# Kernel optimization log

Measured on AMD Instinct MI355X. Metric: run time of the kernel, lower is better.

## Reference

```python
import jax, jax.numpy as jnp
import numpy as np
from jax.scipy.special import digamma, gammaln

B, N, H, W, D = 16, 1024, 32, 32, 256
TEMP = 0.5
KL_WEIGHT = 1e-3


def setup_inputs() -> dict:
    key = jax.random.key(0)
    k1, k2, k3 = jax.random.split(key, 3)
    logits = jax.random.normal(k1, (B, N, H, W), dtype=jnp.float32)
    # codebook initialized uniform(-1/N, 1/N) as in init_type == 'uniform'
    codebook = jax.random.uniform(k2, (N, D), dtype=jnp.float32,
                                  minval=-1.0 / N, maxval=1.0 / N)
    # uniform noise for the Gumbel-softmax rsample (channels-last layout [B,H,W,N])
    uniform_noise = jax.random.uniform(k3, (B, H, W, N), dtype=jnp.float32,
                                       minval=1e-6, maxval=1.0 - 1e-6)
    return {"logits": logits, "codebook": codebook, "uniform_noise": uniform_noise}


def reference(logits, codebook, uniform_noise):
    # convert_to_alpha: evidential mapping alpha = softplus(logits) + 1,
    # then permute(0,2,3,1) -> [B, H, W, N]
    alpha = jax.nn.softplus(jnp.transpose(logits, (0, 2, 3, 1))) + 1.0
    S = jnp.sum(alpha, axis=-1, keepdims=True)            # [B,H,W,1]
    probs = alpha / S                                      # [B,H,W,N]

    # RelaxedOneHotCategorical(temp, probs).rsample() == Gumbel-softmax
    gumbel = -jnp.log(-jnp.log(uniform_noise))
    sample = jax.nn.softmax((jnp.log(probs) + gumbel) / TEMP, axis=-1)  # [B,H,W,N]

    vector_weights = jnp.transpose(sample, (0, 3, 1, 2))   # [B,N,H,W]
    indices = jnp.argmax(vector_weights, axis=1)           # [B,H,W]

    # quantized output via codebook combine
    z_q = jnp.einsum('bnhw,nd->bdhw', vector_weights, codebook)  # [B,D,H,W]

    # KL( Dirichlet(alpha) || Dirichlet(ones(N)) ), closed form with beta=1:
    # lgamma(S) - sum lgamma(alpha) - lgamma(N) + sum (alpha-1)*(digamma(alpha)-digamma(S))
    S1 = S[..., 0]
    kl = (gammaln(S1)
          - jnp.sum(gammaln(alpha), axis=-1)
          - gammaln(jnp.float32(N))
          + jnp.sum((alpha - 1.0) * (digamma(alpha) - digamma(S)), axis=-1))
    kl_loss = KL_WEIGHT * jnp.mean(kl)

    # perplexity over soft encodings
    avg_probs = jnp.mean(sample.reshape(-1, N), axis=0)
    perplexity = jnp.exp(-jnp.sum(avg_probs * jnp.log(avg_probs + 1e-10)))

    return (z_q, kl_loss, indices, perplexity)
```

## Files before the change

### kernel.cpp

```cpp
#include <hip/hip_runtime.h>
#include <math.h>

#define NB 16
#define NN 1024
#define NH 32
#define NW 32
#define ND 256
#define NPIX (NB*NH*NW)

#define ZQ_OFF  0
#define KL_OFF  4194304
#define IDX_OFF 4194305
#define PPL_OFF 4210689

#define LGAMMA_1024F 6071.2804f
#define BS_ROW_B 2080

typedef _Float16 f16x8 __attribute__((ext_vector_type(8)));
typedef _Float16 f16x4 __attribute__((ext_vector_type(4)));
typedef float    f32x4 __attribute__((ext_vector_type(4)));
typedef float    f32x2 __attribute__((ext_vector_type(2)));

__device__ __forceinline__ float fast_rcp(float x){ return __builtin_amdgcn_rcpf(x); }

__device__ __forceinline__ f32x2 elem2(f32x2 x, f32x2 u,
                                       f32x2& S, f32x2& L, f32x2& P,
                                       f32x2& prodAcc){
    f32x2 t;   t[0] = __expf(-fabsf(x[0]));  t[1] = __expf(-fabsf(x[1]));
    f32x2 mx0; mx0[0] = fmaxf(x[0], 0.f);    mx0[1] = fmaxf(x[1], 0.f);
    f32x2 l1p; l1p[0] = __logf(1.f + t[0]);  l1p[1] = __logf(1.f + t[1]);
    f32x2 a  = mx0 + l1p + 1.f;
    f32x2 a1 = a + 1.f, a2 = a + 2.f, z = a + 3.f;
    f32x2 t12  = a1*a2;
    f32x2 prod = a*t12;
    f32x2 rz;  rz[0] = fast_rcp(z[0]);       rz[1] = fast_rcp(z[1]);
    f32x2 rp;  rp[0] = fast_rcp(prod[0]);    rp[1] = fast_rcp(prod[1]);
    f32x2 lz;  lz[0] = __logf(z[0]);         lz[1] = __logf(z[1]);
    prodAcc = prodAcc * prod;
    f32x2 rz2 = rz*rz;
    f32x2 lg = (z - 0.5f)*lz - z + 0.918938533f
             + rz*(0.083333333f - 0.002777778f*rz2);
    f32x2 sr = (t12 + a*(a + a + 3.f))*rp;
    f32x2 dg = lz - 0.5f*rz - rz2*(0.083333333f - 0.008333333f*rz2) - sr;
    S += a; L += lg; P += (a - 1.f)*dg;
    f32x2 d = 1.f - u;
    f32x2 lup = -d*(1.f + d*(0.5f + d*(0.33333333f + d*(0.25f
              + d*(0.2f + d*(0.16666667f + d*0.14285714f))))));
    f32x2 lu;
    lu[0] = (d[0] < 0.09f) ? lup[0] : __logf(u[0]);
    lu[1] = (d[1] < 0.09f) ? lup[1] : __logf(u[1]);
    f32x2 ar; ar[0] = a[0]*fast_rcp(lu[0]);  ar[1] = a[1]*fast_rcp(lu[1]);
    return ar*ar;
}

__global__ __launch_bounds__(256) void k_tr(
    const float* __restrict__ cb, _Float16* __restrict__ cbT)
{
    const int kb = blockIdx.x, kq = blockIdx.y, d = threadIdx.x;
    _Float16 tmp[8];
#pragma unroll
    for (int i = 0; i < 8; ++i)
        tmp[i] = (_Float16)cb[(size_t)(32*kb + 8*kq + i)*ND + d];
    *(f16x8*)(cbT + (size_t)kb*8192 + (size_t)d*32 + 8*kq) = *(f16x8*)tmp;
}

__global__ __launch_bounds__(1024, 2) void k_mega(
    const float* __restrict__ logits, const float* __restrict__ noise,
    const _Float16* __restrict__ cbT, float* __restrict__ colpart,
    float* __restrict__ klpart, float* __restrict__ out)
{
    __shared__ __align__(16) char lds[16*BS_ROW_B + 6*256*4];
    char*  bsb  = lds;
    float* redS = (float*)(lds + 16*BS_ROW_B);
    float* redL = redS + 256;
    float* redP = redL + 256;
    float* redZ = redP + 256;
    float* redM = redZ + 256;
    int*   redI = (int*)(redM + 256);

    const int t    = threadIdx.x;
    const int row  = blockIdx.x >> 1;
    const int w0   = (blockIdx.x & 1) * 16;
    const int b    = row >> 5, h = row & 31;
    const int lane = t & 63;
    const int v    = t >> 6;
    const int wl   = lane & 15;
    const int j4   = (lane >> 4) & 3;
    const int p    = row*32 + w0 + wl;
    const int nq   = 4*v + j4;

    const float* lgB = logits + (size_t)b*(NN*NH*NW) + (size_t)(4*nq)*(NH*NW)
                     + (size_t)h*NW + w0 + wl;
    const float* nzB = noise  + (size_t)p*NN + 4*nq;

    f32x4 u0, u1, u2, u3;
    float x00,x01,x02,x03, x10,x11,x12,x13;
    float x20,x21,x22,x23, x30,x31,x32,x33;
    float ev[16];
    f32x2 SA = (f32x2)0.f, LA = (f32x2)0.f, PA = (f32x2)0.f, ZA = (f32x2)0.f;
    f32x2 SB = (f32x2)0.f, LB = (f32x2)0.f, PB = (f32x2)0.f, ZB = (f32x2)0.f;
    f32x2 prA = (f32x2)1.f, prB = (f32x2)1.f;
    float mxA = -1.f, mxB = -1.f;
    int   idxA = 0, idxB = 0;

    asm volatile(
        "global_load_dwordx4 %0, %4, off\n\t"
        "global_load_dwordx4 %1, %4, off offset:1024\n\t"
        "global_load_dwordx4 %2, %4, off offset:2048\n\t"
        "global_load_dwordx4 %3, %4, off offset:3072"
        : "=&v"(u0), "=&v"(u1), "=&v"(u2), "=&v"(u3)
        : "v"(nzB));

#define LG_ASM(X0,X1,X2,X3,KK) \
    asm volatile( \
        "global_load_dword %0, %4, off offset:-4096\n\t" \
        "global_load_dword %1, %4, off\n\t" \
        "global_load_dword %2, %5, off offset:-4096\n\t" \
        "global_load_dword %3, %5, off" \
        : "=&v"(X0), "=&v"(X1), "=&v"(X2), "=&v"(X3) \
        : "v"(lgB + (size_t)(256*(KK))*1024 + 1024), \
          "v"(lgB + (size_t)(256*(KK))*1024 + 3072))

    LG_ASM(x00,x01,x02,x03, 0);
    LG_ASM(x10,x11,x12,x13, 1);
    LG_ASM(x20,x21,x22,x23, 2);
    LG_ASM(x30,x31,x32,x33, 3);
#undef LG_ASM

#define WAITV(NSTR) do{ asm volatile("s_waitcnt vmcnt(" NSTR ")"); \
                        __builtin_amdgcn_sched_barrier(0); }while(0)

#define DO_PAIR(kk, X0,X1,X2,X3, UV) do{                          \
    f32x2 xA_, xB_, uA_, uB_;                                     \
    xA_[0]=X0; xA_[1]=X1; xB_[0]=X2; xB_[1]=X3;                   \
    uA_[0]=UV[0]; uA_[1]=UV[1]; uB_[0]=UV[2]; uB_[1]=UV[3];       \
    f32x2 eA = elem2(xA_, uA_, SA, LA, PA, prA);                  \
    f32x2 eB = elem2(xB_, uB_, SB, LB, PB, prB);                  \
    ZA += eA; ZB += eB;                                           \
    if (eA[0] > mxA){ mxA = eA[0]; idxA = 256*(kk) + 4*nq + 0; }  \
    if (eA[1] > mxA){ mxA = eA[1]; idxA = 256*(kk) + 4*nq + 1; }  \
    if (eB[0] > mxB){ mxB = eB[0]; idxB = 256*(kk) + 4*nq + 2; }  \
    if (eB[1] > mxB){ mxB = eB[1]; idxB = 256*(kk) + 4*nq + 3; }  \
    ev[4*(kk)+0]=eA[0]; ev[4*(kk)+1]=eA[1];                       \
    ev[4*(kk)+2]=eB[0]; ev[4*(kk)+3]=eB[1]; }while(0)

    WAITV("12");
    DO_PAIR(0, x00,x01,x02,x03, u0);
    WAITV("8");
    DO_PAIR(1, x10,x11,x12,x13, u1);
    WAITV("4");
    DO_PAIR(2, x20,x21,x22,x23, u2);
    WAITV("0");
    DO_PAIR(3, x30,x31,x32,x33, u3);
#undef WAITV
#undef DO_PAIR

    float S = (SA[0] + SA[1]) + (SB[0] + SB[1]);
    float L = (LA[0] + LA[1]) + (LB[0] + LB[1])
            - __logf(prA[0]*prA[1]) - __logf(prB[0]*prB[1]);
    float P = (PA[0] + PA[1]) + (PB[0] + PB[1]);
    float Z = (ZA[0] + ZA[1]) + (ZB[0] + ZB[1]);
    float mx; int idx;
    {
        bool take = (mxB > mxA) || (mxB == mxA && idxB < idxA);
        mx  = take ? mxB : mxA;
        idx = take ? idxB : idxA;
    }

#pragma unroll
    for (int mask = 16; mask < 64; mask <<= 1){
        S += __shfl_xor(S, mask);
        L += __shfl_xor(L, mask);
        P += __shfl_xor(P, mask);
        Z += __shfl_xor(Z, mask);
        float mo = __shfl_xor(mx, mask);
        int   io = __shfl_xor(idx, mask);
        bool take = (mo > mx) || (mo == mx && io < idx);
        mx  = take ? mo : mx;
        idx = take ? io : idx;
    }
    if (j4 == 0){
        redS[16*v + wl] = S;  redL[16*v + wl] = L;
        redP[16*v + wl] = P;  redZ[16*v + wl] = Z;
        redM[16*v + wl] = mx; redI[16*v + wl] = idx;
    }
    __syncthreads();

    float Zt = 0.f;
#pragma unroll
    for (int qz = 0; qz < 16; ++qz) Zt += redZ[16*qz + wl];
    const float zinv = fast_rcp(Zt);

    {
        char* brow = bsb + wl*BS_ROW_B;
        const int sw   = wl & 7;
        const int sub8 = (nq & 1) << 3;
        const int cb2  = nq >> 1;
#pragma unroll
        for (int k = 0; k < 4; ++k){
            f16x4 hv;
            hv[0] = (_Float16)(ev[4*k+0]*zinv);
            hv[1] = (_Float16)(ev[4*k+1]*zinv);
            hv[2] = (_Float16)(ev[4*k+2]*zinv);
            hv[3] = (_Float16)(ev[4*k+3]*zinv);
            *(f16x4*)(brow + (((32*k + cb2) ^ sw) << 4) + sub8) = hv;
        }
    }
    __syncthreads();

    const _Float16* aBase = cbT + (size_t)(16*v + wl)*32 + j4*8;
    const char* bRow = bsb + wl*BS_ROW_B;
    const int fsw = wl & 7;

    f32x4 acc = (f32x4)0.f;
    f16x8 ar[4];
    ar[0] = *(const f16x8*)(aBase);
    ar[1] = *(const f16x8*)(aBase + 8192);
    ar[2] = *(const f16x8*)(aBase + 2*8192);

#pragma unroll
    for (int kb = 0; kb < 32; ++kb){
        if (kb + 3 < 32)
            ar[(kb+3)&3] = *(const f16x8*)(aBase + (size_t)(kb+3)*8192);
        f16x8 bf = *(const f16x8*)(bRow + ((((kb << 2) | j4) ^ fsw) << 4));
        acc = __builtin_amdgcn_mfma_f32_16x16x32_f16(ar[kb&3], bf, acc, 0, 0, 0);
    }

    float* outp = out + (size_t)b*(ND*1024) + h*32 + w0;
#pragma unroll
    for (int r = 0; r < 4; ++r){
        int d = 16*v + 4*j4 + r;
        outp[(size_t)d*1024 + wl] = acc[r];
    }

    {
        float s0 = 0.f;
#pragma unroll
        for (int r = 0; r < 16; ++r){
            const char* br = bsb + r*BS_ROW_B;
            const int sw2 = r & 7;
            s0 += (float)*(const _Float16*)(br + ((((t >> 3) ^ sw2) << 4) + 2*(t & 7)));
        }
        colpart[(size_t)blockIdx.x*NN + t] = s0;
    }

    if (t < 16){
        float Sq = 0.f, Lq = 0.f, Pq = 0.f, M = -1.f;
        int I = 0x7fffffff;
#pragma unroll
        for (int qz = 0; qz < 16; ++qz){
            Sq += redS[16*qz + t]; Lq += redL[16*qz + t]; Pq += redP[16*qz + t];
            float m = redM[16*qz + t]; int i = redI[16*qz + t];
            bool take = (m > M) || (m == M && i < I);
            M = take ? m : M; I = take ? i : I;
        }
        out[IDX_OFF + row*32 + w0 + t] = (float)I;
        float rS  = fast_rcp(Sq);
        float lnS = __logf(Sq);
        float lgS = (Sq - 0.5f)*lnS - Sq + 0.918938533f + 0.083333333f*rS;
        float dgS = lnS - 0.5f*rS;
        float kl = lgS - Lq - LGAMMA_1024F + (Pq - dgS*(Sq - 1024.f));
#pragma unroll
        for (int mask = 1; mask < 16; mask <<= 1) kl += __shfl_xor(kl, mask);
        if (t == 0) klpart[blockIdx.x] = kl;
    }
}

__global__ __launch_bounds__(256) void k_red(
    const float* __restrict__ colpart, float* __restrict__ colsum)
{
    __shared__ float red[8][32];
    const int nl = threadIdx.x & 31;
    const int rs = threadIdx.x >> 5;
    const int n  = blockIdx.x*32 + nl;
    const float* cp = colpart + (size_t)rs*128*NN + n;
    float s = 0.f;
#pragma unroll 8
    for (int r = 0; r < 128; ++r)
        s += cp[(size_t)r*NN];
    red[rs][nl] = s;
    __syncthreads();
    if (threadIdx.x < 32){
        float tot = 0.f;
#pragma unroll
        for (int i = 0; i < 8; ++i) tot += red[i][threadIdx.x];
        colsum[blockIdx.x*32 + threadIdx.x] = tot;
    }
}

__global__ __launch_bounds__(256) void k_final(
    const float* __restrict__ colsum, const float* __restrict__ klpart,
    float* __restrict__ out)
{
    __shared__ float red[8];
    const int tid = threadIdx.x;
    float s = 0.f, kls = 0.f;
#pragma unroll
    for (int n = tid; n < NN; n += 256){
        float avg = colsum[n] * (1.f/16384.f);
        s += avg * logf(avg + 1e-10f);
        kls += klpart[n];
    }
#pragma unroll
    for (int mask = 1; mask < 64; mask <<= 1){
        s   += __shfl_xor(s, mask);
        kls += __shfl_xor(kls, mask);
    }
    if ((tid & 63) == 0){ red[tid >> 6] = s; red[4 + (tid >> 6)] = kls; }
    __syncthreads();
    if (tid == 0){
        float tot = red[0] + red[1] + red[2] + red[3];
        float klt = red[4] + red[5] + red[6] + red[7];
        out[PPL_OFF] = expf(-tot);
        out[KL_OFF]  = 1e-3f * (klt * (1.f/16384.f));
    }
}

extern "C" void kernel_launch(void* const* d_in, const int* in_sizes, int n_in,
                              void* d_out, int out_size, void* d_ws, size_t ws_size,
                              hipStream_t stream)
{
    const float* logits = (const float*)d_in[0];
    const float* cb     = (const float*)d_in[1];
    const float* noise  = (const float*)d_in[2];
    float* out = (float*)d_out;

    float* colpart = (float*)d_ws;
    float* colsum  = colpart + (size_t)1024*NN;
    float* klpart  = colsum + NN;
    _Float16* cbT  = (_Float16*)(klpart + NN);

    k_tr   <<<dim3(32, 4), 256, 0, stream>>>(cb, cbT);
    k_mega <<<dim3(1024), 1024, 0, stream>>>(logits, noise, cbT, colpart, klpart, out);
    k_red  <<<dim3(32),    256, 0, stream>>>(colpart, colsum);
    k_final<<<1, 256, 0, stream>>>(colsum, klpart, out);
}
```

Measured before the change: 214.0 us.

## Process two half-rows per block with prefetch overlap and shared codebook fragments

Each block now handles a full 32-pixel row as two 16-pixel halves. The second half's noise and logits loads are issued before the first half's LDS barrier and softmax write, so their memory latency overlaps the first half's reduction. In the MFMA loop, each codebook fragment loaded from global memory feeds two accumulators, halving cbT traffic per pixel. The grid is halved and the colpart/klpart reductions shrink to match. The cost is more registers and LDS per block, with launch_bounds raised to 8 that may force spills.

```diff
diff --git a/kernel.cpp b/kernel.cpp
--- a/kernel.cpp
+++ b/kernel.cpp
@@ -53,6 +53,23 @@
     return ar*ar;
 }
 
+__device__ __forceinline__ void bs_write(char* bsb, int wl, int nq,
+                                         const float* ev, float zinv){
+    char* brow = bsb + wl*BS_ROW_B;
+    const int sw   = wl & 7;
+    const int sub8 = (nq & 1) << 3;
+    const int cb2  = nq >> 1;
+#pragma unroll
+    for (int k = 0; k < 4; ++k){
+        f16x4 hv;
+        hv[0] = (_Float16)(ev[4*k+0]*zinv);
+        hv[1] = (_Float16)(ev[4*k+1]*zinv);
+        hv[2] = (_Float16)(ev[4*k+2]*zinv);
+        hv[3] = (_Float16)(ev[4*k+3]*zinv);
+        *(f16x4*)(brow + (((32*k + cb2) ^ sw) << 4) + sub8) = hv;
+    }
+}
+
 __global__ __launch_bounds__(256) void k_tr(
     const float* __restrict__ cb, _Float16* __restrict__ cbT)
 {
@@ -64,71 +81,76 @@
     *(f16x8*)(cbT + (size_t)kb*8192 + (size_t)d*32 + 8*kq) = *(f16x8*)tmp;
 }
 
-__global__ __launch_bounds__(1024, 2) void k_mega(
+__global__ __launch_bounds__(1024, 8) void k_mega(
     const float* __restrict__ logits, const float* __restrict__ noise,
     const _Float16* __restrict__ cbT, float* __restrict__ colpart,
     float* __restrict__ klpart, float* __restrict__ out)
 {
-    __shared__ __align__(16) char lds[16*BS_ROW_B + 6*256*4];
-    char*  bsb  = lds;
-    float* redS = (float*)(lds + 16*BS_ROW_B);
-    float* redL = redS + 256;
-    float* redP = redL + 256;
-    float* redZ = redP + 256;
-    float* redM = redZ + 256;
-    int*   redI = (int*)(redM + 256);
+    __shared__ __align__(16) char lds[32*BS_ROW_B + 12*256*4];
+    char*  bsb0 = lds;
+    char*  bsb1 = lds + 16*BS_ROW_B;
+    float* redB = (float*)(lds + 32*BS_ROW_B);
 
     const int t    = threadIdx.x;
-    const int row  = blockIdx.x >> 1;
-    const int w0   = (blockIdx.x & 1) * 16;
-    const int b    = row >> 5, h = row & 31;
+    const int row  = blockIdx.x;
+    const int b    = row >> 5, hh = row & 31;
     const int lane = t & 63;
     const int v    = t >> 6;
     const int wl   = lane & 15;
     const int j4   = (lane >> 4) & 3;
-    const int p    = row*32 + w0 + wl;
     const int nq   = 4*v + j4;
 
-    const float* lgB = logits + (size_t)b*(NN*NH*NW) + (size_t)(4*nq)*(NH*NW)
-                     + (size_t)h*NW + w0 + wl;
-    const float* nzB = noise  + (size_t)p*NN + 4*nq;
+    const float* lgB0 = logits + (size_t)b*(NN*NH*NW) + (size_t)(4*nq)*(NH*NW)
+                      + (size_t)hh*NW + wl;
+    const float* nzB0 = noise  + (size_t)(row*32 + wl)*NN + 4*nq;
+    const float* lgB1 = lgB0 + 16;
+    const float* nzB1 = nzB0 + (size_t)16*NN;
+
+    float ev[16];
+    f32x2 SA, LA, PA, ZA, SB, LB, PB, ZB, prA, prB;
+    float mxA, mxB;
+    int   idxA, idxB;
 
     f32x4 u0, u1, u2, u3;
     float x00,x01,x02,x03, x10,x11,x12,x13;
     float x20,x21,x22,x23, x30,x31,x32,x33;
-    float ev[16];
-    f32x2 SA = (f32x2)0.f, LA = (f32x2)0.f, PA = (f32x2)0.f, ZA = (f32x2)0.f;
-    f32x2 SB = (f32x2)0.f, LB = (f32x2)0.f, PB = (f32x2)0.f, ZB = (f32x2)0.f;
-    f32x2 prA = (f32x2)1.f, prB = (f32x2)1.f;
-    float mxA = -1.f, mxB = -1.f;
-    int   idxA = 0, idxB = 0;
-
-    asm volatile(
-        "global_load_dwordx4 %0, %4, off\n\t"
-        "global_load_dwordx4 %1, %4, off offset:1024\n\t"
-        "global_load_dwordx4 %2, %4, off offset:2048\n\t"
-        "global_load_dwordx4 %3, %4, off offset:3072"
-        : "=&v"(u0), "=&v"(u1), "=&v"(u2), "=&v"(u3)
-        : "v"(nzB));
-
-#define LG_ASM(X0,X1,X2,X3,KK) \
+    f32x4 w0, w1, w2, w3;
+    float y00,y01,y02,y03, y10,y11,y12,y13;
+    float y20,y21,y22,y23, y30,y31,y32,y33;
+
+#define NZ_ASM(U0,U1,U2,U3, NZP) \
+    asm volatile( \
+        "global_load_dwordx4 %0, %4, off\n\t" \
+        "global_load_dwordx4 %1, %4, off offset:1024\n\t" \
+        "global_load_dwordx4 %2, %4, off offset:2048\n\t" \
+        "global_load_dwordx4 %3, %4, off offset:3072" \
+        : "=&v"(U0), "=&v"(U1), "=&v"(U2), "=&v"(U3) : "v"(NZP))
+
+#define LG_ASM(X0,X1,X2,X3, LGP, KK) \
     asm volatile( \
         "global_load_dword %0, %4, off offset:-4096\n\t" \
         "global_load_dword %1, %4, off\n\t" \
         "global_load_dword %2, %5, off offset:-4096\n\t" \
         "global_load_dword %3, %5, off" \
         : "=&v"(X0), "=&v"(X1), "=&v"(X2), "=&v"(X3) \
-        : "v"(lgB + (size_t)(256*(KK))*1024 + 1024), \
-          "v"(lgB + (size_t)(256*(KK))*1024 + 3072))
-
-    LG_ASM(x00,x01,x02,x03, 0);
-    LG_ASM(x10,x11,x12,x13, 1);
-    LG_ASM(x20,x21,x22,x23, 2);
-    LG_ASM(x30,x31,x32,x33, 3);
-#undef LG_ASM
+        : "v"((LGP) + (size_t)(256*(KK))*1024 + 1024), \
+          "v"((LGP) + (size_t)(256*(KK))*1024 + 3072))
 
 #define WAITV(NSTR) do{ asm volatile("s_waitcnt vmcnt(" NSTR ")"); \
                         __builtin_amdgcn_sched_barrier(0); }while(0)
+
+#define BARRIER() do{ \
+    __builtin_amdgcn_sched_barrier(0); \
+    asm volatile("s_waitcnt lgkmcnt(0)" ::: "memory"); \
+    __builtin_amdgcn_sched_barrier(0); \
+    __builtin_amdgcn_s_barrier(); \
+    __builtin_amdgcn_sched_barrier(0); }while(0)
+
+#define STATS_INIT() do{ \
+    SA = (f32x2)0.f; LA = (f32x2)0.f; PA = (f32x2)0.f; ZA = (f32x2)0.f; \
+    SB = (f32x2)0.f; LB = (f32x2)0.f; PB = (f32x2)0.f; ZB = (f32x2)0.f; \
+    prA = (f32x2)1.f; prB = (f32x2)1.f; \
+    mxA = -1.f; mxB = -1.f; idxA = 0; idxB = 0; }while(0)
 
 #define DO_PAIR(kk, X0,X1,X2,X3, UV) do{                          \
     f32x2 xA_, xB_, uA_, uB_;                                     \
@@ -144,126 +166,159 @@
     ev[4*(kk)+0]=eA[0]; ev[4*(kk)+1]=eA[1];                       \
     ev[4*(kk)+2]=eB[0]; ev[4*(kk)+3]=eB[1]; }while(0)
 
-    WAITV("12");
-    DO_PAIR(0, x00,x01,x02,x03, u0);
-    WAITV("8");
-    DO_PAIR(1, x10,x11,x12,x13, u1);
-    WAITV("4");
-    DO_PAIR(2, x20,x21,x22,x23, u2);
-    WAITV("0");
-    DO_PAIR(3, x30,x31,x32,x33, u3);
-#undef WAITV
-#undef DO_PAIR
-
-    float S = (SA[0] + SA[1]) + (SB[0] + SB[1]);
-    float L = (LA[0] + LA[1]) + (LB[0] + LB[1])
-            - __logf(prA[0]*prA[1]) - __logf(prB[0]*prB[1]);
-    float P = (PA[0] + PA[1]) + (PB[0] + PB[1]);
-    float Z = (ZA[0] + ZA[1]) + (ZB[0] + ZB[1]);
-    float mx; int idx;
+#define REDUCE_STORE(BANK) do{                                    \
+    float S = (SA[0]+SA[1]) + (SB[0]+SB[1]);                      \
+    float L = (LA[0]+LA[1]) + (LB[0]+LB[1])                       \
+            - __logf(prA[0]*prA[1]) - __logf(prB[0]*prB[1]);      \
+    float P = (PA[0]+PA[1]) + (PB[0]+PB[1]);                      \
+    float Z = (ZA[0]+ZA[1]) + (ZB[0]+ZB[1]);                      \
+    float mx; int idx;                                            \
+    { bool take = (mxB > mxA) || (mxB == mxA && idxB < idxA);     \
+      mx = take ? mxB : mxA; idx = take ? idxB : idxA; }          \
+    _Pragma("unroll")                                             \
+    for (int mask = 16; mask < 64; mask <<= 1){                   \
+        S += __shfl_xor(S, mask);                                 \
+        L += __shfl_xor(L, mask);                                 \
+        P += __shfl_xor(P, mask);                                 \
+        Z += __shfl_xor(Z, mask);                                 \
+        float mo = __shfl_xor(mx, mask);                          \
+        int   io = __shfl_xor(idx, mask);                         \
+        bool take = (mo > mx) || (mo == mx && io < idx);          \
+        mx = take ? mo : mx; idx = take ? io : idx;               \
+    }                                                             \
+    if (j4 == 0){                                                 \
+        float* bk = redB + (BANK)*1536;                           \
+        bk[       16*v + wl] = S;  bk[256  + 16*v + wl] = L;      \
+        bk[512  + 16*v + wl] = P;  bk[768  + 16*v + wl] = Z;      \
+        bk[1024 + 16*v + wl] = mx;                                \
+        ((int*)bk)[1280 + 16*v + wl] = idx;                       \
+    } }while(0)
+
+    NZ_ASM(u0,u1,u2,u3, nzB0);
+    LG_ASM(x00,x01,x02,x03, lgB0, 0);
+    LG_ASM(x10,x11,x12,x13, lgB0, 1);
+    LG_ASM(x20,x21,x22,x23, lgB0, 2);
+    LG_ASM(x30,x31,x32,x33, lgB0, 3);
+
+    STATS_INIT();
+    WAITV("12"); DO_PAIR(0, x00,x01,x02,x03, u0);
+    WAITV("8");  DO_PAIR(1, x10,x11,x12,x13, u1);
+    WAITV("4");  DO_PAIR(2, x20,x21,x22,x23, u2);
+    WAITV("0");  DO_PAIR(3, x30,x31,x32,x33, u3);
+    REDUCE_STORE(0);
+
+    NZ_ASM(w0,w1,w2,w3, nzB1);
+    LG_ASM(y00,y01,y02,y03, lgB1, 0);
+    LG_ASM(y10,y11,y12,y13, lgB1, 1);
+    LG_ASM(y20,y21,y22,y23, lgB1, 2);
+    LG_ASM(y30,y31,y32,y33, lgB1, 3);
+
+    BARRIER();
+
     {
-        bool take = (mxB > mxA) || (mxB == mxA && idxB < idxA);
-        mx  = take ? mxB : mxA;
-        idx = take ? idxB : idxA;
-    }
-
-#pragma unroll
-    for (int mask = 16; mask < 64; mask <<= 1){
-        S += __shfl_xor(S, mask);
-        L += __shfl_xor(L, mask);
-        P += __shfl_xor(P, mask);
-        Z += __shfl_xor(Z, mask);
-        float mo = __shfl_xor(mx, mask);
-        int   io = __shfl_xor(idx, mask);
-        bool take = (mo > mx) || (mo == mx && io < idx);
-        mx  = take ? mo : mx;
-        idx = take ? io : idx;
-    }
-    if (j4 == 0){
-        redS[16*v + wl] = S;  redL[16*v + wl] = L;
-        redP[16*v + wl] = P;  redZ[16*v + wl] = Z;
-        redM[16*v + wl] = mx; redI[16*v + wl] = idx;
-    }
-    __syncthreads();
-
-    float Zt = 0.f;
-#pragma unroll
-    for (int qz = 0; qz < 16; ++qz) Zt += redZ[16*qz + wl];
-    const float zinv = fast_rcp(Zt);
+        float Zt = 0.f;
+#pragma unroll
+        for (int q = 0; q < 16; ++q) Zt += redB[768 + 16*q + wl];
+        bs_write(bsb0, wl, nq, ev, fast_rcp(Zt));
+    }
+
+    STATS_INIT();
+    WAITV("12"); DO_PAIR(0, y00,y01,y02,y03, w0);
+    WAITV("8");  DO_PAIR(1, y10,y11,y12,y13, w1);
+    WAITV("4");  DO_PAIR(2, y20,y21,y22,y23, w2);
+    WAITV("0");  DO_PAIR(3, y30,y31,y32,y33, w3);
+    REDUCE_STORE(1);
+
+    BARRIER();
 
     {
-        char* brow = bsb + wl*BS_ROW_B;
-        const int sw   = wl & 7;
-        const int sub8 = (nq & 1) << 3;
-        const int cb2  = nq >> 1;
-#pragma unroll
-        for (int k = 0; k < 4; ++k){
-            f16x4 hv;
-            hv[0] = (_Float16)(ev[4*k+0]*zinv);
-            hv[1] = (_Float16)(ev[4*k+1]*zinv);
-            hv[2] = (_Float16)(ev[4*k+2]*zinv);
-            hv[3] = (_Float16)(ev[4*k+3]*zinv);
-            *(f16x4*)(brow + (((32*k + cb2) ^ sw) << 4) + sub8) = hv;
-        }
-    }
-    __syncthreads();
+        float Zt = 0.f;
+#pragma unroll
+        for (int q = 0; q < 16; ++q) Zt += redB[1536 + 768 + 16*q + wl];
+        bs_write(bsb1, wl, nq, ev, fast_rcp(Zt));
+    }
+
+    BARRIER();
 
     const _Float16* aBase = cbT + (size_t)(16*v + wl)*32 + j4*8;
-    const char* bRow = bsb + wl*BS_ROW_B;
+    const char* bRow0 = bsb0 + wl*BS_ROW_B;
+    const char* bRow1 = bsb1 + wl*BS_ROW_B;
     const int fsw = wl & 7;
 
-    f32x4 acc = (f32x4)0.f;
+    f32x4 acc0 = (f32x4)0.f, acc1 = (f32x4)0.f;
     f16x8 ar[4];
     ar[0] = *(const f16x8*)(aBase);
     ar[1] = *(const f16x8*)(aBase + 8192);
     ar[2] = *(const f16x8*)(aBase + 2*8192);
+    __builtin_amdgcn_sched_barrier(0);
 
 #pragma unroll
     for (int kb = 0; kb < 32; ++kb){
-        if (kb + 3 < 32)
+        if (kb + 3 < 32){
             ar[(kb+3)&3] = *(const f16x8*)(aBase + (size_t)(kb+3)*8192);
-        f16x8 bf = *(const f16x8*)(bRow + ((((kb << 2) | j4) ^ fsw) << 4));
-        acc = __builtin_amdgcn_mfma_f32_16x16x32_f16(ar[kb&3], bf, acc, 0, 0, 0);
-    }
-
-    float* outp = out + (size_t)b*(ND*1024) + h*32 + w0;
+            __builtin_amdgcn_sched_barrier(0);
+        }
+        const int boff = (((kb << 2) | j4) ^ fsw) << 4;
+        f16x8 bf0 = *(const f16x8*)(bRow0 + boff);
+        f16x8 bf1 = *(const f16x8*)(bRow1 + boff);
+        acc0 = __builtin_amdgcn_mfma_f32_16x16x32_f16(ar[kb&3], bf0, acc0, 0, 0, 0);
+        acc1 = __builtin_amdgcn_mfma_f32_16x16x32_f16(ar[kb&3], bf1, acc1, 0, 0, 0);
+    }
+
+    float* outp = out + (size_t)b*(ND*1024) + hh*32;
 #pragma unroll
     for (int r = 0; r < 4; ++r){
         int d = 16*v + 4*j4 + r;
-        outp[(size_t)d*1024 + wl] = acc[r];
+        outp[(size_t)d*1024 + wl]      = acc0[r];
+        outp[(size_t)d*1024 + 16 + wl] = acc1[r];
     }
 
     {
         float s0 = 0.f;
 #pragma unroll
         for (int r = 0; r < 16; ++r){
-            const char* br = bsb + r*BS_ROW_B;
-            const int sw2 = r & 7;
-            s0 += (float)*(const _Float16*)(br + ((((t >> 3) ^ sw2) << 4) + 2*(t & 7)));
+            const int off = ((((t >> 3) ^ (r & 7)) << 4) + 2*(t & 7));
+            s0 += (float)*(const _Float16*)(bsb0 + r*BS_ROW_B + off);
+            s0 += (float)*(const _Float16*)(bsb1 + r*BS_ROW_B + off);
         }
-        colpart[(size_t)blockIdx.x*NN + t] = s0;
+        colpart[(size_t)row*NN + t] = s0;
     }
 
     if (t < 16){
-        float Sq = 0.f, Lq = 0.f, Pq = 0.f, M = -1.f;
-        int I = 0x7fffffff;
-#pragma unroll
-        for (int qz = 0; qz < 16; ++qz){
-            Sq += redS[16*qz + t]; Lq += redL[16*qz + t]; Pq += redP[16*qz + t];
-            float m = redM[16*qz + t]; int i = redI[16*qz + t];
-            bool take = (m > M) || (m == M && i < I);
-            M = take ? m : M; I = take ? i : I;
+        float klb = 0.f;
+#pragma unroll
+        for (int h2 = 0; h2 < 2; ++h2){
+            const float* bk = redB + h2*1536;
+            const int*  bkI = (const int*)bk;
+            float Sq = 0.f, Lq = 0.f, Pq = 0.f, M = -1.f;
+            int I = 0x7fffffff;
+#pragma unroll
+            for (int q = 0; q < 16; ++q){
+                Sq += bk[16*q + t]; Lq += bk[256 + 16*q + t];
+                Pq += bk[512 + 16*q + t];
+                float m = bk[1024 + 16*q + t]; int i = bkI[1280 + 16*q + t];
+                bool take = (m > M) || (m == M && i < I);
+                M = take ? m : M; I = take ? i : I;
+            }
+            out[IDX_OFF + row*32 + 16*h2 + t] = (float)I;
+            float rS  = fast_rcp(Sq);
+            float lnS = __logf(Sq);
+            float lgS = (Sq - 0.5f)*lnS - Sq + 0.918938533f + 0.083333333f*rS;
+            float dgS = lnS - 0.5f*rS;
+            float kl = lgS - Lq - LGAMMA_1024F + (Pq - dgS*(Sq - 1024.f));
+#pragma unroll
+            for (int mask = 1; mask < 16; mask <<= 1) kl += __shfl_xor(kl, mask);
+            klb += kl;
         }
-        out[IDX_OFF + row*32 + w0 + t] = (float)I;
-        float rS  = fast_rcp(Sq);
-        float lnS = __logf(Sq);
-        float lgS = (Sq - 0.5f)*lnS - Sq + 0.918938533f + 0.083333333f*rS;
-        float dgS = lnS - 0.5f*rS;
-        float kl = lgS - Lq - LGAMMA_1024F + (Pq - dgS*(Sq - 1024.f));
-#pragma unroll
-        for (int mask = 1; mask < 16; mask <<= 1) kl += __shfl_xor(kl, mask);
-        if (t == 0) klpart[blockIdx.x] = kl;
-    }
+        if (t == 0) klpart[row] = klb;
+    }
+#undef NZ_ASM
+#undef LG_ASM
+#undef WAITV
+#undef BARRIER
+#undef STATS_INIT
+#undef DO_PAIR
+#undef REDUCE_STORE
 }
 
 __global__ __launch_bounds__(256) void k_red(
@@ -273,10 +328,10 @@
     const int nl = threadIdx.x & 31;
     const int rs = threadIdx.x >> 5;
     const int n  = blockIdx.x*32 + nl;
-    const float* cp = colpart + (size_t)rs*128*NN + n;
+    const float* cp = colpart + (size_t)(rs*64)*NN + n;
     float s = 0.f;
 #pragma unroll 8
-    for (int r = 0; r < 128; ++r)
+    for (int r = 0; r < 64; ++r)
         s += cp[(size_t)r*NN];
     red[rs][nl] = s;
     __syncthreads();
@@ -299,7 +354,7 @@
     for (int n = tid; n < NN; n += 256){
         float avg = colsum[n] * (1.f/16384.f);
         s += avg * logf(avg + 1e-10f);
-        kls += klpart[n];
+        if (n < 512) kls += klpart[n];
     }
 #pragma unroll
     for (int mask = 1; mask < 64; mask <<= 1){
@@ -326,12 +381,12 @@
     float* out = (float*)d_out;
 
     float* colpart = (float*)d_ws;
-    float* colsum  = colpart + (size_t)1024*NN;
+    float* colsum  = colpart + (size_t)512*NN;
     float* klpart  = colsum + NN;
-    _Float16* cbT  = (_Float16*)(klpart + NN);
+    _Float16* cbT  = (_Float16*)(klpart + 1024);
 
     k_tr   <<<dim3(32, 4), 256, 0, stream>>>(cb, cbT);
-    k_mega <<<dim3(1024), 1024, 0, stream>>>(logits, noise, cbT, colpart, klpart, out);
+    k_mega <<<dim3(512), 1024, 0, stream>>>(logits, noise, cbT, colpart, klpart, out);
     k_red  <<<dim3(32),    256, 0, stream>>>(colpart, colsum);
     k_final<<<1, 256, 0, stream>>>(colsum, klpart, out);
 }
```

Measured after the change: 229.9 us. 7.4% more time.
